# Optimization experiments

Hardware: AMD Instinct MI355X
Metric: run time of the kernel (lower is better)

Reference implementation:

```python
import jax, jax.numpy as jnp
import numpy as np
from jax import lax

BN_EPS = 1e-5

# Straight-through-estimator sign (XNOR-Net BinActive): fwd=sign, bwd=clipped identity
@jax.custom_vjp
def ste_sign(x):
    return jnp.sign(x)

def _ste_fwd(x):
    return jnp.sign(x), x

def _ste_bwd(x, g):
    return (g * (jnp.abs(x) <= 1.0).astype(g.dtype),)

ste_sign.defvjp(_ste_fwd, _ste_bwd)

def conv2d(x, w):
    # x: NCHW, w: OIHW, stride 1, VALID
    return lax.conv_general_dilated(x, w, (1, 1), 'VALID',
                                    dimension_numbers=('NCHW', 'OIHW', 'NCHW'))

def maxpool2(x):
    return lax.reduce_window(x, -jnp.inf, lax.max, (1, 1, 2, 2), (1, 1, 2, 2), 'VALID')

def bn2d(x, gamma, beta):
    # training-mode BatchNorm2d: batch stats over (N,H,W), biased variance
    mean = jnp.mean(x, axis=(0, 2, 3), keepdims=True)
    var = jnp.mean((x - mean) ** 2, axis=(0, 2, 3), keepdims=True)
    xhat = (x - mean) * lax.rsqrt(var + BN_EPS)
    return xhat * gamma[None, :, None, None] + beta[None, :, None, None]

def bn1d(x, gamma, beta):
    mean = jnp.mean(x, axis=0, keepdims=True)
    var = jnp.mean((x - mean) ** 2, axis=0, keepdims=True)
    xhat = (x - mean) * lax.rsqrt(var + BN_EPS)
    return xhat * gamma[None, :] + beta[None, :]

def bin_conv2d(x, w):
    # XNOR-style: binarize input and weight, scale by per-filter alpha = mean|W|
    alpha = jnp.mean(jnp.abs(w), axis=(1, 2, 3))  # [O]
    out = conv2d(ste_sign(x), ste_sign(w))
    return out * alpha[None, :, None, None]

def bin_linear(x, w):
    # w: [out_features, in_features]
    alpha = jnp.mean(jnp.abs(w), axis=1)  # [out_features]
    return (ste_sign(x) @ ste_sign(w).T) * alpha[None, :]


def setup_inputs() -> dict:
    key = jax.random.key(0)
    ks = jax.random.split(key, 8)
    B = 8192
    inp = {
        'x': jax.random.normal(ks[0], (B, 1, 28, 28), dtype=jnp.float32),
        'conv1_w': jax.random.normal(ks[1], (20, 1, 5, 5), dtype=jnp.float32) * 0.2,
        'bn1_g': jnp.ones((20,), jnp.float32),
        'bn1_b': jnp.zeros((20,), jnp.float32),
        'conv2_w': jax.random.normal(ks[2], (50, 20, 5, 5), dtype=jnp.float32) * 0.04,
        'bn2_g': jnp.ones((50,), jnp.float32),
        'bn2_b': jnp.zeros((50,), jnp.float32),
        'fc1_w': jax.random.normal(ks[3], (500, 800), dtype=jnp.float32) * 0.035,
        'bn3_g': jnp.ones((500,), jnp.float32),
        'bn3_b': jnp.zeros((500,), jnp.float32),
        'fc2_w': jax.random.normal(ks[4], (10, 500), dtype=jnp.float32) * 0.045,
        'fc2_b': jnp.zeros((10,), jnp.float32),
    }
    return inp


def reference(x, conv1_w, bn1_g, bn1_b, conv2_w, bn2_g, bn2_b,
              fc1_w, bn3_g, bn3_b, fc2_w, fc2_b):
    h = conv2d(x, conv1_w)                 # [B,20,24,24]
    h = jax.nn.relu(bn2d(h, bn1_g, bn1_b))
    h = maxpool2(h)                        # [B,20,12,12]
    h = bin_conv2d(h, conv2_w)             # [B,50,8,8]
    h = jax.nn.relu(bn2d(h, bn2_g, bn2_b))
    h = maxpool2(h)                        # [B,50,4,4]
    h = h.reshape(-1, 50 * 4 * 4)          # [B,800]
    h = bin_linear(h, fc1_w)               # [B,500]
    h = jax.nn.relu(bn1d(h, bn3_g, bn3_b))
    return h @ fc2_w.T + fc2_b[None, :]    # [B,10]
```

## Files before the change

kernel.cpp:

```cpp
#include <hip/hip_runtime.h>
#include <stdint.h>

#define BATCH 8192
#define NJOB  1179648

__global__ __launch_bounds__(256) void k_pack(const float* __restrict__ w2,
    const float* __restrict__ w3, unsigned* __restrict__ wpos2,
    unsigned* __restrict__ wneg2, float* __restrict__ alpha2,
    unsigned* __restrict__ wpos3, unsigned* __restrict__ wneg3,
    float* __restrict__ alpha3, int* __restrict__ flags2, int* __restrict__ flags3){
  __shared__ int zf;
  int tid = threadIdx.x;
  if (tid == 0) zf = 0;
  __syncthreads();
  if (blockIdx.x < 5){
    int t = blockIdx.x*256 + tid;
    int had0 = 0;
    if (t < 1250){
      int o = t/25, k = t%25;
      unsigned p=0, n=0;
      for (int i=0;i<20;i++){
        float v = w2[(o*20+i)*25 + k];
        if (v > 0.f) p |= 1u<<i;
        else if (v < 0.f) n |= 1u<<i;
        else had0 = 1;
      }
      wpos2[t] = p; wneg2[t] = n;
    }
    if (t < 50){
      float s = 0.f;
      for (int i=0;i<500;i++) s += fabsf(w2[t*500+i]);
      alpha2[t] = s / 500.f;
    }
    if (had0) atomicOr(&zf, 1);
    __syncthreads();
    if (tid == 0) flags2[blockIdx.x] = zf;
  } else {
    int t = (blockIdx.x-5)*256 + tid;
    int had0 = 0;
    if (t < 12500){
      int j = t/25, w = t%25;
      unsigned p=0, n=0;
      for (int bb=0;bb<32;bb++){
        float v = w3[j*800 + w*32 + bb];
        if (v > 0.f) p |= 1u<<bb;
        else if (v < 0.f) n |= 1u<<bb;
        else had0 = 1;
      }
      wpos3[t] = p; wneg3[t] = n;
    }
    if (t < 500){
      float s = 0.f;
      for (int i=0;i<800;i++) s += fabsf(w3[t*800+i]);
      alpha3[t] = s / 800.f;
    }
    if (had0) atomicOr(&zf, 1);
    __syncthreads();
    if (tid == 0) flags3[blockIdx.x-5] = zf;
  }
}


#define CONV1_ROWS(IPTR)                                                      \
  float vA0=0.f,vA1=0.f,vA2=0.f,vA3=0.f;                                      \
  float vB0=0.f,vB1=0.f,vB2=0.f,vB3=0.f;                                      \
  _Pragma("unroll")                                                           \
  for (int r=0;r<6;r++){                                                      \
    const float2* rp = (const float2*)((IPTR) + r*28);                        \
    float2 p0 = rp[0], p1 = rp[1], p2 = rp[2];                                \
    float row0=p0.x, row1=p0.y, row2=p1.x, row3=p1.y, row4=p2.x, row5=p2.y;   \
    if (r<5){                                                                 \
      _Pragma("unroll")                                                       \
      for (int kx=0;kx<5;kx++){                                               \
        float e0 = (kx==0?row0:kx==1?row1:kx==2?row2:kx==3?row3:row4);        \
        float e1 = (kx==0?row1:kx==1?row2:kx==2?row3:kx==3?row4:row5);        \
        float w = wa[r*5+kx], u = wb[r*5+kx];                                 \
        vA0=fmaf(e0,w,vA0); vA1=fmaf(e1,w,vA1);                               \
        vB0=fmaf(e0,u,vB0); vB1=fmaf(e1,u,vB1);                               \
      }                                                                       \
    }                                                                         \
    if (r>0){                                                                 \
      _Pragma("unroll")                                                       \
      for (int kx=0;kx<5;kx++){                                               \
        float e0 = (kx==0?row0:kx==1?row1:kx==2?row2:kx==3?row3:row4);        \
        float e1 = (kx==0?row1:kx==1?row2:kx==2?row3:kx==3?row4:row5);        \
        float w = wa[(r-1)*5+kx], u = wb[(r-1)*5+kx];                         \
        vA2=fmaf(e0,w,vA2); vA3=fmaf(e1,w,vA3);                               \
        vB2=fmaf(e0,u,vB2); vB3=fmaf(e1,u,vB3);                               \
      }                                                                       \
    }                                                                         \
  }

template<bool STORE_MM>
__global__ __launch_bounds__(256) void k_conv1_stats(const float* __restrict__ x,
        const float* __restrict__ w1, float* __restrict__ part1,
        float4* __restrict__ c1mm){
  __shared__ float img[8*784];
  __shared__ float wsh[500];
  __shared__ float red[4][40];
  int tid = threadIdx.x;
  size_t base = (size_t)blockIdx.x * 8;
  const float4* xv = (const float4*)(x + base*784);
  float4* iv = (float4*)img;
  for (int i=tid;i<1568;i+=256) iv[i] = xv[i];
  for (int i=tid;i<500;i+=256)  wsh[i] = w1[i];
  __syncthreads();
  int lane = tid & 63, wid = tid >> 6;
#pragma unroll 1
  for (int cg=0; cg<10; ++cg){
    float wa[25], wb[25];
#pragma unroll
    for (int k=0;k<25;k++){ wa[k]=wsh[(2*cg)*25+k]; wb[k]=wsh[(2*cg+1)*25+k]; }
    float sa=0.f, qa=0.f, sb=0.f, qb=0.f;
#pragma unroll 1
    for (int job=tid; job<8*144; job+=256){
      int li = job/144, pp = job%144;
      int py = pp/12, px = pp%12;
      const float* ip = &img[li*784 + py*56 + px*2];
      CONV1_ROWS(ip)
      sa += (vA0+vA1)+(vA2+vA3);
      qa = fmaf(vA0,vA0, fmaf(vA1,vA1, fmaf(vA2,vA2, fmaf(vA3,vA3, qa))));
      sb += (vB0+vB1)+(vB2+vB3);
      qb = fmaf(vB0,vB0, fmaf(vB1,vB1, fmaf(vB2,vB2, fmaf(vB3,vB3, qb))));
      if (STORE_MM){
        float mxA = fmaxf(fmaxf(vA0,vA1),fmaxf(vA2,vA3));
        float mnA = fminf(fminf(vA0,vA1),fminf(vA2,vA3));
        float mxB = fmaxf(fmaxf(vB0,vB1),fmaxf(vB2,vB3));
        float mnB = fminf(fminf(vB0,vB1),fminf(vB2,vB3));
        c1mm[(size_t)cg*NJOB + (base+li)*144 + pp] = make_float4(mxA,mnA,mxB,mnB);
      }
    }
#pragma unroll
    for (int d=32; d>0; d>>=1){
      sa += __shfl_down(sa,d); qa += __shfl_down(qa,d);
      sb += __shfl_down(sb,d); qb += __shfl_down(qb,d);
    }
    if (lane==0){
      red[wid][(2*cg)*2]   = sa; red[wid][(2*cg)*2+1]   = qa;
      red[wid][(2*cg+1)*2] = sb; red[wid][(2*cg+1)*2+1] = qb;
    }
  }
  __syncthreads();
  if (tid < 40)
    part1[blockIdx.x*40 + tid] = red[0][tid]+red[1][tid]+red[2][tid]+red[3][tid];
}

__global__ __launch_bounds__(256) void k_reduce1(const float* __restrict__ part1,
        const float* __restrict__ g, const float* __restrict__ b,
        float* __restrict__ s1t1){
  __shared__ double rs[256], rq[256];
  int c = blockIdx.x;
  int tid = threadIdx.x;
  double s=0.0, q=0.0;
  for (int i=tid;i<1024;i+=256){
    s += (double)part1[i*40 + c*2];
    q += (double)part1[i*40 + c*2 + 1];
  }
  rs[tid]=s; rq[tid]=q;
  __syncthreads();
  for (int d=128; d>0; d>>=1){
    if (tid<d){ rs[tid]+=rs[tid+d]; rq[tid]+=rq[tid+d]; }
    __syncthreads();
  }
  if (tid==0){
    double N = 8192.0*576.0;
    double mean = rs[0]/N, var = rq[0]/N - mean*mean;
    double r = 1.0/sqrt(var + 1e-5);
    double sc = (double)g[c]*r;
    s1t1[c*2]   = (float)sc;
    s1t1[c*2+1] = (float)((double)b[c] - mean*sc);
  }
}

__global__ __launch_bounds__(256) void k_conv1_bin(const float* __restrict__ x,
        const float* __restrict__ w1, const float* __restrict__ s1t1,
        unsigned* __restrict__ mask1){
  __shared__ float img[8*784];
  __shared__ float wsh[500];
  __shared__ float st[40];
  __shared__ unsigned lw[8*144];
  int tid = threadIdx.x;
  size_t base = (size_t)blockIdx.x * 8;
  const float4* xv = (const float4*)(x + base*784);
  float4* iv = (float4*)img;
  for (int i=tid;i<1568;i+=256) iv[i] = xv[i];
  for (int i=tid;i<500;i+=256)  wsh[i] = w1[i];
  for (int i=tid;i<8*144;i+=256) lw[i] = 0u;
  if (tid < 40) st[tid] = s1t1[tid];
  __syncthreads();
#pragma unroll 1
  for (int cg=0; cg<10; ++cg){
    float wa[25], wb[25];
#pragma unroll
    for (int k=0;k<25;k++){ wa[k]=wsh[(2*cg)*25+k]; wb[k]=wsh[(2*cg+1)*25+k]; }
    float sA = st[(2*cg)*2],   tA = st[(2*cg)*2+1];
    float sB = st[(2*cg+1)*2], tB = st[(2*cg+1)*2+1];
#pragma unroll 1
    for (int job=tid; job<8*144; job+=256){
      int li = job/144, pp = job%144;
      int py = pp/12, px = pp%12;
      const float* ip = &img[li*784 + py*56 + px*2];
      CONV1_ROWS(ip)
      unsigned bA = (fmaf(vA0,sA,tA) > 0.f) || (fmaf(vA1,sA,tA) > 0.f) ||
                    (fmaf(vA2,sA,tA) > 0.f) || (fmaf(vA3,sA,tA) > 0.f);
      unsigned bB = (fmaf(vB0,sB,tB) > 0.f) || (fmaf(vB1,sB,tB) > 0.f) ||
                    (fmaf(vB2,sB,tB) > 0.f) || (fmaf(vB3,sB,tB) > 0.f);
      lw[job] |= (bA << (2*cg)) | (bB << (2*cg+1));
    }
  }
  __syncthreads();
  for (int i=tid;i<8*144;i+=256){
    int li = i/144, pp = i%144;
    mask1[(base+li)*144 + pp] = lw[i];
  }
}

__global__ __launch_bounds__(256) void k_conv1_bin_lite(const float4* __restrict__ c1mm,
        const float* __restrict__ s1t1, unsigned* __restrict__ mask1){
  __shared__ float st[40];
  int tid = threadIdx.x;
  if (tid < 40) st[tid] = s1t1[tid];
  __syncthreads();
  int J = blockIdx.x*256 + tid;
  unsigned word = 0;
#pragma unroll
  for (int cg=0; cg<10; ++cg){
    float4 v = c1mm[(size_t)cg*NJOB + J];
    float sA = st[4*cg+0], tA = st[4*cg+1];
    float sB = st[4*cg+2], tB = st[4*cg+3];
    float vA = (sA > 0.f) ? v.x : v.y;
    float vB = (sB > 0.f) ? v.z : v.w;
    word |= ((fmaf(vA,sA,tA) > 0.f) ? 1u : 0u) << (2*cg);
    word |= ((fmaf(vB,sB,tB) > 0.f) ? 1u : 0u) << (2*cg+1);
  }
  mask1[J] = word;
}

template<bool STORE_S>
__global__ __launch_bounds__(256) void k_conv2_stats(const unsigned* __restrict__ mask1,
    const unsigned* __restrict__ wpos, const unsigned* __restrict__ wneg,
    const int* __restrict__ flags2, int* __restrict__ part2, short* __restrict__ S16){
  __shared__ unsigned m1[4*144];
  __shared__ __align__(16) unsigned wp[1400], wn[1400];
  __shared__ int red[4][100];
  int tid = threadIdx.x;
  size_t base = (size_t)blockIdx.x * 4;
  bool slow = (flags2[0]|flags2[1]|flags2[2]|flags2[3]|flags2[4]) != 0;
  for (int i=tid;i<4*144;i+=256) m1[i] = mask1[base*144 + i];
  for (int i=tid;i<1400;i+=256){
    int o = i/28, k = i%28;
    wn[i] = (k<25) ? wneg[o*25+k] : 0u;
    if (slow) wp[i] = (k<25) ? wpos[o*25+k] : 0u;
  }
  __syncthreads();
  int lane = tid & 63, wid = tid >> 6;
  int y2 = lane >> 3, x2 = lane & 7;
  unsigned mw[28];
  const unsigned* mrow = &m1[wid*144];
#pragma unroll
  for (int ky=0;ky<5;ky++)
#pragma unroll
    for (int kx=0;kx<5;kx++)
      mw[ky*5+kx] = mrow[(y2+ky)*12 + x2+kx];
  mw[25]=0u; mw[26]=0u; mw[27]=0u;
  if (!slow){
    int pbase = 0;
#pragma unroll
    for (int k=0;k<25;k++) pbase += __popc(mw[k]);
#pragma unroll 1
    for (int o=0;o<50;o++){
      const uint4* n4 = (const uint4*)&wn[o*28];
      int Sn=0;
#pragma unroll
      for (int g=0; g<7; g++){
        uint4 N = n4[g];
        Sn += __popc(mw[4*g]&N.x) + __popc(mw[4*g+1]&N.y)
            + __popc(mw[4*g+2]&N.z) + __popc(mw[4*g+3]&N.w);
      }
      int S = pbase - 2*Sn;
      if (STORE_S) S16[((base+wid)*50 + o)*64 + lane] = (short)S;
      int rs = S, rq = S*S;
#pragma unroll
      for (int d=32; d>0; d>>=1){ rs += __shfl_down(rs,d); rq += __shfl_down(rq,d); }
      if (lane==0){ red[wid][o*2] = rs; red[wid][o*2+1] = rq; }
    }
  } else {
#pragma unroll 1
    for (int o=0;o<50;o++){
      const uint4* p4 = (const uint4*)&wp[o*28];
      const uint4* n4 = (const uint4*)&wn[o*28];
      int Sp=0, Sn=0;
#pragma unroll
      for (int g=0; g<7; g++){
        uint4 P = p4[g], N = n4[g];
        Sp += __popc(mw[4*g]&P.x) + __popc(mw[4*g+1]&P.y)
            + __popc(mw[4*g+2]&P.z) + __popc(mw[4*g+3]&P.w);
        Sn += __popc(mw[4*g]&N.x) + __popc(mw[4*g+1]&N.y)
            + __popc(mw[4*g+2]&N.z) + __popc(mw[4*g+3]&N.w);
      }
      int S = Sp - Sn;
      if (STORE_S) S16[((base+wid)*50 + o)*64 + lane] = (short)S;
      int rs = S, rq = S*S;
#pragma unroll
      for (int d=32; d>0; d>>=1){ rs += __shfl_down(rs,d); rq += __shfl_down(rq,d); }
      if (lane==0){ red[wid][o*2] = rs; red[wid][o*2+1] = rq; }
    }
  }
  __syncthreads();
  if (tid < 100)
    part2[blockIdx.x*100 + tid] = red[0][tid]+red[1][tid]+red[2][tid]+red[3][tid];
}

__global__ __launch_bounds__(256) void k_reduce2(const int* __restrict__ part2,
        const float* __restrict__ alpha2, const float* __restrict__ g,
        const float* __restrict__ b, float* __restrict__ s2t2){
  __shared__ long long rs[256], rq[256];
  int o = blockIdx.x;
  int tid = threadIdx.x;
  long long s=0, q=0;
  for (int i=tid;i<2048;i+=256){
    s += part2[i*100 + o*2];
    q += part2[i*100 + o*2 + 1];
  }
  rs[tid]=s; rq[tid]=q;
  __syncthreads();
  for (int d=128; d>0; d>>=1){
    if (tid<d){ rs[tid]+=rs[tid+d]; rq[tid]+=rq[tid+d]; }
    __syncthreads();
  }
  if (tid==0){
    double N = 8192.0*64.0;
    double meanS = (double)rs[0]/N, E2 = (double)rq[0]/N;
    double varS = E2 - meanS*meanS;
    double a = (double)alpha2[o];
    double mean_g = a*meanS, var_g = a*a*varS;
    double r = 1.0/sqrt(var_g + 1e-5);
    double sc = (double)g[o]*r;
    s2t2[o*2]   = (float)(sc*a);
    s2t2[o*2+1] = (float)((double)b[o] - mean_g*sc);
  }
}

#define BIN2_POOL_BODY                                                        \
    unsigned long long bal = __ballot(cond);                                  \
    unsigned long long t4 = bal | (bal>>1) | (bal>>8) | (bal>>9);             \
    bool pb = (lane < 16) && ((t4 >> (16*(lane>>2) + 2*(lane&3))) & 1ull);    \
    unsigned long long bal2 = __ballot(pb);                                   \
    if (lane==0){                                                             \
      unsigned pooled16 = (unsigned)(bal2 & 0xFFFFull);                       \
      lw[wid*25 + (o>>1)] |= pooled16 << (16*(o&1));                          \
    }

__global__ __launch_bounds__(256) void k_bin2(const unsigned* __restrict__ mask1,
    const unsigned* __restrict__ wpos, const unsigned* __restrict__ wneg,
    const float* __restrict__ s2t2, unsigned* __restrict__ mask2){
  __shared__ unsigned m1[4*144];
  __shared__ __align__(16) unsigned wp[1400], wn[1400];
  __shared__ float st[100];
  __shared__ unsigned lw[100];
  int tid = threadIdx.x;
  size_t base = (size_t)blockIdx.x * 4;
  for (int i=tid;i<4*144;i+=256) m1[i] = mask1[base*144 + i];
  for (int i=tid;i<1400;i+=256){
    int o = i/28, k = i%28;
    wp[i] = (k<25) ? wpos[o*25+k] : 0u;
    wn[i] = (k<25) ? wneg[o*25+k] : 0u;
  }
  if (tid < 100){ st[tid] = s2t2[tid]; lw[tid] = 0u; }
  __syncthreads();
  int lane = tid & 63, wid = tid >> 6;
  int y2 = lane >> 3, x2 = lane & 7;
  unsigned mw[28];
  const unsigned* mrow = &m1[wid*144];
#pragma unroll
  for (int ky=0;ky<5;ky++)
#pragma unroll
    for (int kx=0;kx<5;kx++)
      mw[ky*5+kx] = mrow[(y2+ky)*12 + x2+kx];
  mw[25]=0u; mw[26]=0u; mw[27]=0u;
#pragma unroll 1
  for (int o=0;o<50;o++){
    const uint4* p4 = (const uint4*)&wp[o*28];
    const uint4* n4 = (const uint4*)&wn[o*28];
    int Sp=0, Sn=0;
#pragma unroll
    for (int g=0; g<7; g++){
      uint4 P = p4[g], N = n4[g];
      Sp += __popc(mw[4*g]&P.x) + __popc(mw[4*g+1]&P.y)
          + __popc(mw[4*g+2]&P.z) + __popc(mw[4*g+3]&P.w);
      Sn += __popc(mw[4*g]&N.x) + __popc(mw[4*g+1]&N.y)
          + __popc(mw[4*g+2]&N.z) + __popc(mw[4*g+3]&N.w);
    }
    int S = Sp - Sn;
    bool cond = fmaf((float)S, st[o*2], st[o*2+1]) > 0.f;
    BIN2_POOL_BODY
  }
  __syncthreads();
  if (tid < 100) mask2[base*25 + tid] = lw[tid];
}

__global__ __launch_bounds__(256) void k_bin2_lite(const short* __restrict__ S16,
    const float* __restrict__ s2t2, unsigned* __restrict__ mask2){
  __shared__ float st[100];
  __shared__ unsigned lw[100];
  int tid = threadIdx.x;
  if (tid < 100){ st[tid] = s2t2[tid]; lw[tid] = 0u; }
  __syncthreads();
  int lane = tid & 63, wid = tid >> 6;
  size_t img = (size_t)blockIdx.x*4 + wid;
#pragma unroll 1
  for (int o=0;o<50;o++){
    int S = S16[(img*50 + o)*64 + lane];
    bool cond = fmaf((float)S, st[o*2], st[o*2+1]) > 0.f;
    BIN2_POOL_BODY
  }
  __syncthreads();
  if (tid < 100) mask2[blockIdx.x*100 + tid] = lw[tid];
}

__global__ __launch_bounds__(256) void k_fc1(const unsigned* __restrict__ mask2,
    const unsigned* __restrict__ wpos, const unsigned* __restrict__ wneg,
    const int* __restrict__ flags3, short* __restrict__ S3){
  __shared__ unsigned m2s[8*25];
  __shared__ short s3s[8*500];
  int tid = threadIdx.x;
  size_t base = (size_t)blockIdx.x * 8;
  for (int i=tid;i<200;i+=256) m2s[i] = mask2[base*25 + i];
  __syncthreads();
  int f = 0;
  for (int i=0;i<49;i++) f |= flags3[i];
  int bl = tid & 7;
  int jg = tid >> 3;
  const unsigned* mrow = &m2s[bl*25];
  if (f == 0){
    int pbase = 0;
#pragma unroll
    for (int w=0;w<25;w++) pbase += __popc(mrow[w]);
#pragma unroll 1
    for (int j=jg; j<500; j+=32){
      const unsigned* n = &wneg[j*25];
      int Sn = 0;
#pragma unroll
      for (int w=0;w<25;w++) Sn += __popc(mrow[w] & n[w]);
      s3s[bl*500 + j] = (short)(pbase - 2*Sn);
    }
  } else {
#pragma unroll 1
    for (int j=jg; j<500; j+=32){
      const unsigned* p = &wpos[j*25];
      const unsigned* n = &wneg[j*25];
      int S = 0;
#pragma unroll
      for (int w=0;w<25;w++){
        unsigned m = mrow[w];
        S += __popc(m & p[w]) - __popc(m & n[w]);
      }
      s3s[bl*500 + j] = (short)S;
    }
  }
  __syncthreads();
  for (int i=tid;i<8*500;i+=256) S3[base*500 + i] = s3s[i];
}

__global__ __launch_bounds__(256) void k_stats3(const short* __restrict__ S3,
                                                int* __restrict__ part3){
  int tid = threadIdx.x;
  const short* p = &S3[(size_t)blockIdx.x * 64 * 500];
  int s0=0,q0=0,s1=0,q1=0;
  for (int b=0;b<64;b++){
    int v0 = p[b*500 + tid];
    s0 += v0; q0 += v0*v0;
    if (tid < 244){
      int v1 = p[b*500 + tid + 256];
      s1 += v1; q1 += v1*v1;
    }
  }
  part3[blockIdx.x*1000 + tid*2]     = s0;
  part3[blockIdx.x*1000 + tid*2 + 1] = q0;
  if (tid < 244){
    part3[blockIdx.x*1000 + (tid+256)*2]     = s1;
    part3[blockIdx.x*1000 + (tid+256)*2 + 1] = q1;
  }
}

__global__ void k_reduce3(const int* __restrict__ part3, const float* __restrict__ alpha3,
                          const float* __restrict__ g, const float* __restrict__ b,
                          float* __restrict__ s3t3){
  int j = blockIdx.x*256 + threadIdx.x;
  if (j >= 500) return;
  long long s=0, q=0;
  for (int i=0;i<128;i++){
    s += part3[i*1000 + j*2];
    q += part3[i*1000 + j*2 + 1];
  }
  double N = 8192.0;
  double meanS = (double)s/N, E2 = (double)q/N;
  double varS = E2 - meanS*meanS;
  double a = (double)alpha3[j];
  double mean_u = a*meanS, var_u = a*a*varS;
  double r = 1.0/sqrt(var_u + 1e-5);
  double sc = (double)g[j]*r;
  s3t3[j*2]   = (float)(sc*a);
  s3t3[j*2+1] = (float)((double)b[j] - mean_u*sc);
}

__global__ __launch_bounds__(256) void k_final(const short* __restrict__ S3,
    const float* __restrict__ s3t3, const float* __restrict__ fc2w,
    const float* __restrict__ fc2b, float* __restrict__ out){
  __shared__ float w[5000];
  __shared__ float st[1000];
  __shared__ float bias[10];
  int tid = threadIdx.x;
  for (int i=tid;i<5000;i+=256) w[i] = fc2w[i];
  for (int i=tid;i<1000;i+=256) st[i] = s3t3[i];
  if (tid<10) bias[tid] = fc2b[tid];
  __syncthreads();
  int sub = tid & 7;
  int li  = tid >> 3;
  size_t b = (size_t)blockIdx.x*32 + li;
  const short* sp = &S3[b*500];
  float acc[10];
#pragma unroll
  for (int m=0;m<10;m++) acc[m] = 0.f;
#pragma unroll 1
  for (int j=sub; j<500; j+=8){
    float h = fmaf((float)sp[j], st[j*2], st[j*2+1]);
    h = fmaxf(h, 0.f);
#pragma unroll
    for (int m=0;m<10;m++) acc[m] = fmaf(h, w[m*500+j], acc[m]);
  }
#pragma unroll
  for (int m=0;m<10;m++){
    float v = acc[m];
    v += __shfl_xor(v, 1);
    v += __shfl_xor(v, 2);
    v += __shfl_xor(v, 4);
    acc[m] = v;
  }
  if (sub == 0){
#pragma unroll
    for (int m=0;m<10;m++) out[b*10 + m] = acc[m] + bias[m];
  }
}

extern "C" void kernel_launch(void* const* d_in, const int* in_sizes, int n_in,
                              void* d_out, int out_size, void* d_ws, size_t ws_size,
                              hipStream_t stream){
  const float* x    = (const float*)d_in[0];
  const float* w1   = (const float*)d_in[1];
  const float* bn1g = (const float*)d_in[2];
  const float* bn1b = (const float*)d_in[3];
  const float* w2   = (const float*)d_in[4];
  const float* bn2g = (const float*)d_in[5];
  const float* bn2b = (const float*)d_in[6];
  const float* w3   = (const float*)d_in[7];
  const float* bn3g = (const float*)d_in[8];
  const float* bn3b = (const float*)d_in[9];
  const float* w4   = (const float*)d_in[10];
  const float* b4   = (const float*)d_in[11];
  float* out = (float*)d_out;
  (void)in_sizes; (void)n_in; (void)out_size;

  char* wsb = (char*)d_ws;
  size_t off = 0;
  auto alloc = [&](size_t n){ size_t o = off; off = (off + n + 255) & ~(size_t)255; return o; };
  float*    s1t1   = (float*)(wsb + alloc(40*sizeof(float)));
  float*    s2t2   = (float*)(wsb + alloc(100*sizeof(float)));
  float*    s3t3   = (float*)(wsb + alloc(1000*sizeof(float)));
  float*    alpha2 = (float*)(wsb + alloc(50*sizeof(float)));
  float*    alpha3 = (float*)(wsb + alloc(500*sizeof(float)));
  int*      flags2 = (int*)(wsb + alloc(5*4));
  int*      flags3 = (int*)(wsb + alloc(49*4));
  unsigned* wpos2  = (unsigned*)(wsb + alloc(1250*4));
  unsigned* wneg2  = (unsigned*)(wsb + alloc(1250*4));
  unsigned* wpos3  = (unsigned*)(wsb + alloc(12500*4));
  unsigned* wneg3  = (unsigned*)(wsb + alloc(12500*4));
  float*    part1  = (float*)(wsb + alloc(1024*40*4));
  int*      part2  = (int*)(wsb + alloc(2048*100*4));
  int*      part3  = (int*)(wsb + alloc(128*1000*4));
  unsigned* mask1  = (unsigned*)(wsb + alloc((size_t)BATCH*144*4));
  unsigned* mask2  = (unsigned*)(wsb + alloc((size_t)BATCH*25*4));
  short*    S3     = (short*)(wsb + alloc((size_t)BATCH*500*2));
  short*    S16    = (short*)(wsb + alloc((size_t)BATCH*50*64*2));
  bool useS16 = (ws_size >= off);
  float4*   c1mm   = (float4*)(wsb + alloc((size_t)10*NJOB*16));
  bool useMM  = (ws_size >= off);

  hipLaunchKernelGGL(k_pack, dim3(54), dim3(256), 0, stream,
                     w2, w3, wpos2, wneg2, alpha2, wpos3, wneg3, alpha3, flags2, flags3);
  if (useMM)
    hipLaunchKernelGGL(HIP_KERNEL_NAME(k_conv1_stats<true>),  dim3(1024), dim3(256), 0, stream, x, w1, part1, c1mm);
  else
    hipLaunchKernelGGL(HIP_KERNEL_NAME(k_conv1_stats<false>), dim3(1024), dim3(256), 0, stream, x, w1, part1, c1mm);
  hipLaunchKernelGGL(k_reduce1,      dim3(20),    dim3(256), 0, stream, part1, bn1g, bn1b, s1t1);
  if (useMM)
    hipLaunchKernelGGL(k_conv1_bin_lite, dim3(4608), dim3(256), 0, stream, c1mm, s1t1, mask1);
  else
    hipLaunchKernelGGL(k_conv1_bin,  dim3(1024),  dim3(256), 0, stream, x, w1, s1t1, mask1);
  if (useS16)
    hipLaunchKernelGGL(HIP_KERNEL_NAME(k_conv2_stats<true>),  dim3(2048), dim3(256), 0, stream, mask1, wpos2, wneg2, flags2, part2, S16);
  else
    hipLaunchKernelGGL(HIP_KERNEL_NAME(k_conv2_stats<false>), dim3(2048), dim3(256), 0, stream, mask1, wpos2, wneg2, flags2, part2, S16);
  hipLaunchKernelGGL(k_reduce2,      dim3(50),    dim3(256), 0, stream, part2, alpha2, bn2g, bn2b, s2t2);
  if (useS16)
    hipLaunchKernelGGL(k_bin2_lite,  dim3(2048),  dim3(256), 0, stream, S16, s2t2, mask2);
  else
    hipLaunchKernelGGL(k_bin2,       dim3(2048),  dim3(256), 0, stream, mask1, wpos2, wneg2, s2t2, mask2);
  hipLaunchKernelGGL(k_fc1,          dim3(1024),  dim3(256), 0, stream, mask2, wpos3, wneg3, flags3, S3);
  hipLaunchKernelGGL(k_stats3,       dim3(128),   dim3(256), 0, stream, S3, part3);
  hipLaunchKernelGGL(k_reduce3,      dim3(2),     dim3(256), 0, stream, part3, alpha3, bn3g, bn3b, s3t3);
  hipLaunchKernelGGL(k_final,        dim3(256),   dim3(256), 0, stream, S3, s3t3, w4, b4, out);
}
```

Baseline: 328.9 us.

## Halve conv1 extremum buffer by gamma-sign select; split conv2 stats into separate pass

Conv1 stats now uses the sign of the BN gamma to keep only the relevant extremum per channel. It stores a float2 instead of a float4, halving the intermediate write and read traffic. Conv2 no longer does per-output shuffle reductions inline; a separate k_stats2 kernel reads S16 back to compute sums and squares, and the 25th tap is handled with a scalar popcount instead of padded zero words. This adds an extra launch and an extra read of S16 in exchange for a lighter conv2 inner loop. The gamma-sign selection assumes rsqrt(var) is positive, so the scale's sign matches gamma's.

```diff
diff --git a/kernel.cpp b/kernel.cpp
--- a/kernel.cpp
+++ b/kernel.cpp
@@ -93,10 +93,11 @@
 
 template<bool STORE_MM>
 __global__ __launch_bounds__(256) void k_conv1_stats(const float* __restrict__ x,
-        const float* __restrict__ w1, float* __restrict__ part1,
-        float4* __restrict__ c1mm){
+        const float* __restrict__ w1, const float* __restrict__ g1,
+        float* __restrict__ part1, float2* __restrict__ c1ext){
   __shared__ float img[8*784];
   __shared__ float wsh[500];
+  __shared__ float gsh[20];
   __shared__ float red[4][40];
   int tid = threadIdx.x;
   size_t base = (size_t)blockIdx.x * 8;
@@ -104,6 +105,7 @@
   float4* iv = (float4*)img;
   for (int i=tid;i<1568;i+=256) iv[i] = xv[i];
   for (int i=tid;i<500;i+=256)  wsh[i] = w1[i];
+  if (tid < 20) gsh[tid] = g1[tid];
   __syncthreads();
   int lane = tid & 63, wid = tid >> 6;
 #pragma unroll 1
@@ -111,6 +113,7 @@
     float wa[25], wb[25];
 #pragma unroll
     for (int k=0;k<25;k++){ wa[k]=wsh[(2*cg)*25+k]; wb[k]=wsh[(2*cg+1)*25+k]; }
+    float gA = gsh[2*cg], gB = gsh[2*cg+1];
     float sa=0.f, qa=0.f, sb=0.f, qb=0.f;
 #pragma unroll 1
     for (int job=tid; job<8*144; job+=256){
@@ -127,7 +130,9 @@
         float mnA = fminf(fminf(vA0,vA1),fminf(vA2,vA3));
         float mxB = fmaxf(fmaxf(vB0,vB1),fmaxf(vB2,vB3));
         float mnB = fminf(fminf(vB0,vB1),fminf(vB2,vB3));
-        c1mm[(size_t)cg*NJOB + (base+li)*144 + pp] = make_float4(mxA,mnA,mxB,mnB);
+        float eA = (gA > 0.f) ? mxA : mnA;
+        float eB = (gB > 0.f) ? mxB : mnB;
+        c1ext[(size_t)cg*NJOB + (base+li)*144 + pp] = make_float2(eA,eB);
       }
     }
 #pragma unroll
@@ -215,7 +220,7 @@
   }
 }
 
-__global__ __launch_bounds__(256) void k_conv1_bin_lite(const float4* __restrict__ c1mm,
+__global__ __launch_bounds__(256) void k_conv1_bin_lite(const float2* __restrict__ c1ext,
         const float* __restrict__ s1t1, unsigned* __restrict__ mask1){
   __shared__ float st[40];
   int tid = threadIdx.x;
@@ -225,24 +230,20 @@
   unsigned word = 0;
 #pragma unroll
   for (int cg=0; cg<10; ++cg){
-    float4 v = c1mm[(size_t)cg*NJOB + J];
+    float2 v = c1ext[(size_t)cg*NJOB + J];
     float sA = st[4*cg+0], tA = st[4*cg+1];
     float sB = st[4*cg+2], tB = st[4*cg+3];
-    float vA = (sA > 0.f) ? v.x : v.y;
-    float vB = (sB > 0.f) ? v.z : v.w;
-    word |= ((fmaf(vA,sA,tA) > 0.f) ? 1u : 0u) << (2*cg);
-    word |= ((fmaf(vB,sB,tB) > 0.f) ? 1u : 0u) << (2*cg+1);
+    word |= ((fmaf(v.x,sA,tA) > 0.f) ? 1u : 0u) << (2*cg);
+    word |= ((fmaf(v.y,sB,tB) > 0.f) ? 1u : 0u) << (2*cg+1);
   }
   mask1[J] = word;
 }
 
-template<bool STORE_S>
-__global__ __launch_bounds__(256) void k_conv2_stats(const unsigned* __restrict__ mask1,
+__global__ __launch_bounds__(256) void k_conv2(const unsigned* __restrict__ mask1,
     const unsigned* __restrict__ wpos, const unsigned* __restrict__ wneg,
-    const int* __restrict__ flags2, int* __restrict__ part2, short* __restrict__ S16){
+    const int* __restrict__ flags2, short* __restrict__ S16){
   __shared__ unsigned m1[4*144];
   __shared__ __align__(16) unsigned wp[1400], wn[1400];
-  __shared__ int red[4][100];
   int tid = threadIdx.x;
   size_t base = (size_t)blockIdx.x * 4;
   bool slow = (flags2[0]|flags2[1]|flags2[2]|flags2[3]|flags2[4]) != 0;
@@ -255,14 +256,14 @@
   __syncthreads();
   int lane = tid & 63, wid = tid >> 6;
   int y2 = lane >> 3, x2 = lane & 7;
-  unsigned mw[28];
+  unsigned mw[25];
   const unsigned* mrow = &m1[wid*144];
 #pragma unroll
   for (int ky=0;ky<5;ky++)
 #pragma unroll
     for (int kx=0;kx<5;kx++)
       mw[ky*5+kx] = mrow[(y2+ky)*12 + x2+kx];
-  mw[25]=0u; mw[26]=0u; mw[27]=0u;
+  short* sp = &S16[((base+wid)*50)*64 + lane];
   if (!slow){
     int pbase = 0;
 #pragma unroll
@@ -272,17 +273,13 @@
       const uint4* n4 = (const uint4*)&wn[o*28];
       int Sn=0;
 #pragma unroll
-      for (int g=0; g<7; g++){
+      for (int g=0; g<6; g++){
         uint4 N = n4[g];
         Sn += __popc(mw[4*g]&N.x) + __popc(mw[4*g+1]&N.y)
             + __popc(mw[4*g+2]&N.z) + __popc(mw[4*g+3]&N.w);
       }
-      int S = pbase - 2*Sn;
-      if (STORE_S) S16[((base+wid)*50 + o)*64 + lane] = (short)S;
-      int rs = S, rq = S*S;
-#pragma unroll
-      for (int d=32; d>0; d>>=1){ rs += __shfl_down(rs,d); rq += __shfl_down(rq,d); }
-      if (lane==0){ red[wid][o*2] = rs; red[wid][o*2+1] = rq; }
+      Sn += __popc(mw[24] & wn[o*28+24]);
+      sp[o*64] = (short)(pbase - 2*Sn);
     }
   } else {
 #pragma unroll 1
@@ -291,20 +288,99 @@
       const uint4* n4 = (const uint4*)&wn[o*28];
       int Sp=0, Sn=0;
 #pragma unroll
-      for (int g=0; g<7; g++){
+      for (int g=0; g<6; g++){
         uint4 P = p4[g], N = n4[g];
         Sp += __popc(mw[4*g]&P.x) + __popc(mw[4*g+1]&P.y)
             + __popc(mw[4*g+2]&P.z) + __popc(mw[4*g+3]&P.w);
         Sn += __popc(mw[4*g]&N.x) + __popc(mw[4*g+1]&N.y)
             + __popc(mw[4*g+2]&N.z) + __popc(mw[4*g+3]&N.w);
       }
-      int S = Sp - Sn;
-      if (STORE_S) S16[((base+wid)*50 + o)*64 + lane] = (short)S;
-      int rs = S, rq = S*S;
-#pragma unroll
-      for (int d=32; d>0; d>>=1){ rs += __shfl_down(rs,d); rq += __shfl_down(rq,d); }
-      if (lane==0){ red[wid][o*2] = rs; red[wid][o*2+1] = rq; }
-    }
+      Sp += __popc(mw[24] & wp[o*28+24]);
+      Sn += __popc(mw[24] & wn[o*28+24]);
+      sp[o*64] = (short)(Sp - Sn);
+    }
+  }
+}
+
+__global__ __launch_bounds__(256) void k_stats2(const short* __restrict__ S16,
+        int* __restrict__ part2){
+  int tid = threadIdx.x;
+  int lane = tid & 63, wid = tid >> 6;
+  const short* p = S16 + (size_t)blockIdx.x * 32 * 3200;
+  int rs[13], rq[13];
+#pragma unroll
+  for (int k=0;k<13;k++){ rs[k]=0; rq[k]=0; }
+#pragma unroll 1
+  for (int im=0; im<32; ++im){
+    const short* q = p + im*3200 + tid;
+#pragma unroll
+    for (int k=0;k<13;k++){
+      if (wid + 4*k < 50){
+        int v = q[256*k];
+        rs[k] += v; rq[k] += v*v;
+      }
+    }
+  }
+#pragma unroll
+  for (int k=0;k<13;k++){
+    int o = wid + 4*k;
+    if (o < 50){
+      int s = rs[k], q2 = rq[k];
+#pragma unroll
+      for (int d=32; d>0; d>>=1){ s += __shfl_down(s,d); q2 += __shfl_down(q2,d); }
+      if (lane==0){
+        part2[blockIdx.x*100 + o*2]     = s;
+        part2[blockIdx.x*100 + o*2 + 1] = q2;
+      }
+    }
+  }
+}
+
+__global__ __launch_bounds__(256) void k_conv2_stats_legacy(const unsigned* __restrict__ mask1,
+    const unsigned* __restrict__ wpos, const unsigned* __restrict__ wneg,
+    const int* __restrict__ flags2, int* __restrict__ part2){
+  __shared__ unsigned m1[4*144];
+  __shared__ __align__(16) unsigned wp[1400], wn[1400];
+  __shared__ int red[4][100];
+  int tid = threadIdx.x;
+  size_t base = (size_t)blockIdx.x * 4;
+  bool slow = (flags2[0]|flags2[1]|flags2[2]|flags2[3]|flags2[4]) != 0;
+  for (int i=tid;i<4*144;i+=256) m1[i] = mask1[base*144 + i];
+  for (int i=tid;i<1400;i+=256){
+    int o = i/28, k = i%28;
+    wn[i] = (k<25) ? wneg[o*25+k] : 0u;
+    wp[i] = (k<25) ? wpos[o*25+k] : 0u;
+  }
+  __syncthreads();
+  int lane = tid & 63, wid = tid >> 6;
+  int y2 = lane >> 3, x2 = lane & 7;
+  unsigned mw[25];
+  const unsigned* mrow = &m1[wid*144];
+#pragma unroll
+  for (int ky=0;ky<5;ky++)
+#pragma unroll
+    for (int kx=0;kx<5;kx++)
+      mw[ky*5+kx] = mrow[(y2+ky)*12 + x2+kx];
+#pragma unroll 1
+  for (int o=0;o<50;o++){
+    const uint4* p4 = (const uint4*)&wp[o*28];
+    const uint4* n4 = (const uint4*)&wn[o*28];
+    int Sp=0, Sn=0;
+#pragma unroll
+    for (int g=0; g<6; g++){
+      uint4 P = p4[g], N = n4[g];
+      Sp += __popc(mw[4*g]&P.x) + __popc(mw[4*g+1]&P.y)
+          + __popc(mw[4*g+2]&P.z) + __popc(mw[4*g+3]&P.w);
+      Sn += __popc(mw[4*g]&N.x) + __popc(mw[4*g+1]&N.y)
+          + __popc(mw[4*g+2]&N.z) + __popc(mw[4*g+3]&N.w);
+    }
+    Sp += __popc(mw[24] & wp[o*28+24]);
+    Sn += __popc(mw[24] & wn[o*28+24]);
+    int S = Sp - Sn;
+    int rs = S, rq = S*S;
+#pragma unroll
+    for (int d=32; d>0; d>>=1){ rs += __shfl_down(rs,d); rq += __shfl_down(rq,d); }
+    if (lane==0){ red[wid][o*2] = rs; red[wid][o*2+1] = rq; }
   }
   __syncthreads();
   if (tid < 100)
@@ -312,13 +388,13 @@
 }
 
 __global__ __launch_bounds__(256) void k_reduce2(const int* __restrict__ part2,
-        const float* __restrict__ alpha2, const float* __restrict__ g,
+        int nchunk, const float* __restrict__ alpha2, const float* __restrict__ g,
         const float* __restrict__ b, float* __restrict__ s2t2){
   __shared__ long long rs[256], rq[256];
   int o = blockIdx.x;
   int tid = threadIdx.x;
   long long s=0, q=0;
-  for (int i=tid;i<2048;i+=256){
+  for (int i=tid;i<nchunk;i+=256){
     s += part2[i*100 + o*2];
     q += part2[i*100 + o*2 + 1];
   }
@@ -370,27 +446,28 @@
   __syncthreads();
   int lane = tid & 63, wid = tid >> 6;
   int y2 = lane >> 3, x2 = lane & 7;
-  unsigned mw[28];
+  unsigned mw[25];
   const unsigned* mrow = &m1[wid*144];
 #pragma unroll
   for (int ky=0;ky<5;ky++)
 #pragma unroll
     for (int kx=0;kx<5;kx++)
       mw[ky*5+kx] = mrow[(y2+ky)*12 + x2+kx];
-  mw[25]=0u; mw[26]=0u; mw[27]=0u;
 #pragma unroll 1
   for (int o=0;o<50;o++){
     const uint4* p4 = (const uint4*)&wp[o*28];
     const uint4* n4 = (const uint4*)&wn[o*28];
     int Sp=0, Sn=0;
 #pragma unroll
-    for (int g=0; g<7; g++){
+    for (int g=0; g<6; g++){
       uint4 P = p4[g], N = n4[g];
       Sp += __popc(mw[4*g]&P.x) + __popc(mw[4*g+1]&P.y)
           + __popc(mw[4*g+2]&P.z) + __popc(mw[4*g+3]&P.w);
       Sn += __popc(mw[4*g]&N.x) + __popc(mw[4*g+1]&N.y)
           + __popc(mw[4*g+2]&N.z) + __popc(mw[4*g+3]&N.w);
     }
+    Sp += __popc(mw[24] & wp[o*28+24]);
+    Sn += __popc(mw[24] & wn[o*28+24]);
     int S = Sp - Sn;
     bool cond = fmaf((float)S, st[o*2], st[o*2+1]) > 0.f;
     BIN2_POOL_BODY
@@ -583,29 +660,30 @@
   short*    S3     = (short*)(wsb + alloc((size_t)BATCH*500*2));
   short*    S16    = (short*)(wsb + alloc((size_t)BATCH*50*64*2));
   bool useS16 = (ws_size >= off);
-  float4*   c1mm   = (float4*)(wsb + alloc((size_t)10*NJOB*16));
+  float2*   c1ext  = (float2*)(wsb + alloc((size_t)10*NJOB*8));
   bool useMM  = (ws_size >= off);
 
   hipLaunchKernelGGL(k_pack, dim3(54), dim3(256), 0, stream,
                      w2, w3, wpos2, wneg2, alpha2, wpos3, wneg3, alpha3, flags2, flags3);
   if (useMM)
-    hipLaunchKernelGGL(HIP_KERNEL_NAME(k_conv1_stats<true>),  dim3(1024), dim3(256), 0, stream, x, w1, part1, c1mm);
+    hipLaunchKernelGGL(HIP_KERNEL_NAME(k_conv1_stats<true>),  dim3(1024), dim3(256), 0, stream, x, w1, bn1g, part1, c1ext);
   else
-    hipLaunchKernelGGL(HIP_KERNEL_NAME(k_conv1_stats<false>), dim3(1024), dim3(256), 0, stream, x, w1, part1, c1mm);
+    hipLaunchKernelGGL(HIP_KERNEL_NAME(k_conv1_stats<false>), dim3(1024), dim3(256), 0, stream, x, w1, bn1g, part1, c1ext);
   hipLaunchKernelGGL(k_reduce1,      dim3(20),    dim3(256), 0, stream, part1, bn1g, bn1b, s1t1);
   if (useMM)
-    hipLaunchKernelGGL(k_conv1_bin_lite, dim3(4608), dim3(256), 0, stream, c1mm, s1t1, mask1);
+    hipLaunchKernelGGL(k_conv1_bin_lite, dim3(4608), dim3(256), 0, stream, c1ext, s1t1, mask1);
   else
     hipLaunchKernelGGL(k_conv1_bin,  dim3(1024),  dim3(256), 0, stream, x, w1, s1t1, mask1);
-  if (useS16)
-    hipLaunchKernelGGL(HIP_KERNEL_NAME(k_conv2_stats<true>),  dim3(2048), dim3(256), 0, stream, mask1, wpos2, wneg2, flags2, part2, S16);
-  else
-    hipLaunchKernelGGL(HIP_KERNEL_NAME(k_conv2_stats<false>), dim3(2048), dim3(256), 0, stream, mask1, wpos2, wneg2, flags2, part2, S16);
-  hipLaunchKernelGGL(k_reduce2,      dim3(50),    dim3(256), 0, stream, part2, alpha2, bn2g, bn2b, s2t2);
-  if (useS16)
+  if (useS16){
+    hipLaunchKernelGGL(k_conv2,      dim3(2048),  dim3(256), 0, stream, mask1, wpos2, wneg2, flags2, S16);
+    hipLaunchKernelGGL(k_stats2,     dim3(256),   dim3(256), 0, stream, S16, part2);
+    hipLaunchKernelGGL(k_reduce2,    dim3(50),    dim3(256), 0, stream, part2, 256, alpha2, bn2g, bn2b, s2t2);
     hipLaunchKernelGGL(k_bin2_lite,  dim3(2048),  dim3(256), 0, stream, S16, s2t2, mask2);
-  else
+  } else {
+    hipLaunchKernelGGL(k_conv2_stats_legacy, dim3(2048), dim3(256), 0, stream, mask1, wpos2, wneg2, flags2, part2);
+    hipLaunchKernelGGL(k_reduce2,    dim3(50),    dim3(256), 0, stream, part2, 2048, alpha2, bn2g, bn2b, s2t2);
     hipLaunchKernelGGL(k_bin2,       dim3(2048),  dim3(256), 0, stream, mask1, wpos2, wneg2, s2t2, mask2);
+  }
   hipLaunchKernelGGL(k_fc1,          dim3(1024),  dim3(256), 0, stream, mask2, wpos3, wneg3, flags3, S3);
   hipLaunchKernelGGL(k_stats3,       dim3(128),   dim3(256), 0, stream, S3, part3);
   hipLaunchKernelGGL(k_reduce3,      dim3(2),     dim3(256), 0, stream, part3, alpha3, bn3g, bn3b, s3t3);
```

Result: no change. 327.3 us (-0.5%).
